# Performance work log

Hardware: AMD Instinct MI355X
Metric: run time of the kernel (lower is better)

The kernel has to match this reference:

```python
import jax, jax.numpy as jnp
import numpy as np

# Config: AydinConfig(hidden_dim=1024, intermediate_dim=2048, num_experts=8, top_k=2)
E, H, I, K = 8, 1024, 2048, 2
B, S = 4, 2048


def setup_inputs() -> dict:
    key = jax.random.key(0)
    k1, k2, k3, k4 = jax.random.split(key, 4)
    x = jax.random.normal(k1, (B, S, H), dtype=jnp.float32)
    # nn.Linear(H, E, bias=False): weight shape (E, H), default init ~ U(-1/sqrt(H), 1/sqrt(H))
    router_w = jax.random.uniform(k2, (E, H), dtype=jnp.float32,
                                  minval=-1.0, maxval=1.0) / np.sqrt(H).astype(np.float32)
    # normal init, std=0.02 (reset_parameters)
    w13 = jax.random.normal(k3, (E, H, 2 * I), dtype=jnp.float32) * 0.02
    w2 = jax.random.normal(k4, (E, I, H), dtype=jnp.float32) * 0.02
    return {"x": x, "router_w": router_w, "w13": w13, "w2": w2}


def reference(x, router_w, w13, w2):
    # Router: logits (B,S,E) -> softmax -> top-k with renormalized weights
    logits = jnp.einsum('bsh,eh->bse', x, router_w)
    probs = jax.nn.softmax(logits, axis=-1)
    weights, indices = jax.lax.top_k(probs, K)            # (B,S,K)
    weights = weights / (weights.sum(axis=-1, keepdims=True) + 1e-6)
    # Expert SwiGLU, computed densely over all experts then gathered.
    # Same math as the torch per-token weight gather, but avoids the
    # (B,S,K,H,2I) gathered-weight blowup.
    h13 = jnp.einsum('bsh,ehi->bsei', x, w13)             # (B,S,E,2I)
    gate, up = jnp.split(h13, 2, axis=-1)                 # (B,S,E,I) each
    h = jax.nn.silu(gate) * up
    y = jnp.einsum('bsei,eih->bseh', h, w2)               # (B,S,E,H)
    # Gather top-k expert outputs and combine with routing weights
    y_sel = jnp.take_along_axis(y, indices[..., None], axis=2)  # (B,S,K,H)
    return (y_sel * weights[..., None]).sum(axis=2)       # (B,S,H)
```

## Files before the change

### kernel.cpp

```cpp
#include <hip/hip_runtime.h>
#include <hip/hip_bf16.h>
#include <math.h>

#define NEXP 8
#define HD 1024
#define ID 2048
#define NTOK 8192
#define NROWS 16384

typedef __bf16 bf16_t;
typedef __bf16 bf16x8 __attribute__((ext_vector_type(8)));
typedef float f32x4 __attribute__((ext_vector_type(4)));

#define BM 128
#define BK 32
#define MAXT 160

__device__ __forceinline__ void gl16(const void* g, void* l) {
    __builtin_amdgcn_global_load_lds(
        (const __attribute__((address_space(1))) unsigned int*)g,
        (__attribute__((address_space(3))) unsigned int*)l, 16, 0, 0);
}

__global__ __launch_bounds__(256)
void router_kernel(const float* __restrict__ x, const float* __restrict__ rw,
                   bf16_t* __restrict__ xb, int* __restrict__ topk_idx,
                   float* __restrict__ topk_w)
{
    const int t = blockIdx.x;
    const int tid = threadIdx.x;
    const float4 xv = ((const float4*)(x + (size_t)t * HD))[tid];
    float acc[NEXP];
#pragma unroll
    for (int e = 0; e < NEXP; ++e) {
        const float4 w4 = ((const float4*)(rw + e * HD))[tid];
        acc[e] = xv.x * w4.x + xv.y * w4.y + xv.z * w4.z + xv.w * w4.w;
    }
    bf16_t tmp[4] = {(bf16_t)xv.x, (bf16_t)xv.y, (bf16_t)xv.z, (bf16_t)xv.w};
    *(uint2*)(xb + (size_t)t * HD + tid * 4) = *(const uint2*)tmp;

    __shared__ float red[4][NEXP];
    const int lane = tid & 63, wv = tid >> 6;
#pragma unroll
    for (int e = 0; e < NEXP; ++e) {
        float v = acc[e];
#pragma unroll
        for (int off = 32; off >= 1; off >>= 1) v += __shfl_down(v, off, 64);
        if (lane == 0) red[wv][e] = v;
    }
    __syncthreads();
    if (tid == 0) {
        float lg[NEXP], mx = -1e30f;
#pragma unroll
        for (int e = 0; e < NEXP; ++e) {
            lg[e] = red[0][e] + red[1][e] + red[2][e] + red[3][e];
            mx = fmaxf(mx, lg[e]);
        }
        float p[NEXP], s = 0.f;
#pragma unroll
        for (int e = 0; e < NEXP; ++e) { p[e] = __expf(lg[e] - mx); s += p[e]; }
        const float inv = 1.f / s;
#pragma unroll
        for (int e = 0; e < NEXP; ++e) p[e] *= inv;
        int i0 = 0; float p0 = p[0];
#pragma unroll
        for (int e = 1; e < NEXP; ++e) if (p[e] > p0) { p0 = p[e]; i0 = e; }
        int i1 = -1; float p1 = -1.f;
#pragma unroll
        for (int e = 0; e < NEXP; ++e) if (e != i0 && p[e] > p1) { p1 = p[e]; i1 = e; }
        const float d = 1.f / (p0 + p1 + 1e-6f);
        topk_idx[t * 2 + 0] = i0; topk_idx[t * 2 + 1] = i1;
        topk_w[t * 2 + 0] = p0 * d; topk_w[t * 2 + 1] = p1 * d;
    }
}

__global__ __launch_bounds__(256)
void count_kernel(const int* __restrict__ topk_idx, int* __restrict__ counts)
{
    __shared__ int lc[NEXP];
    const int tid = threadIdx.x;
    if (tid < NEXP) lc[tid] = 0;
    __syncthreads();
    const int t = blockIdx.x * 256 + tid;
    atomicAdd(&lc[topk_idx[t * 2 + 0]], 1);
    atomicAdd(&lc[topk_idx[t * 2 + 1]], 1);
    __syncthreads();
    if (tid < NEXP) atomicAdd(&counts[tid], lc[tid]);
}

__global__ void scan_kernel(const int* __restrict__ counts, int* __restrict__ offsets,
                            int* __restrict__ cursor, unsigned* __restrict__ tile_map)
{
    __shared__ int tb[NEXP + 1];
    if (threadIdx.x == 0) {
        int s = 0, tacc = 0;
        for (int e = 0; e < NEXP; ++e) {
            offsets[e] = s; cursor[e] = s; s += counts[e];
            tb[e] = tacc; tacc += (counts[e] + BM - 1) / BM;
        }
        tb[NEXP] = tacc;
    }
    __syncthreads();
    for (int i = threadIdx.x; i < MAXT; i += 64) {
        unsigned v = 0xFFFFFFFFu;
#pragma unroll
        for (int e = 0; e < NEXP; ++e)
            if (i >= tb[e] && i < tb[e + 1]) v = ((unsigned)e << 16) | (unsigned)(i - tb[e]);
        tile_map[i] = v;
    }
}

__global__ __launch_bounds__(256)
void scatter_kernel(const int* __restrict__ topk_idx, const float* __restrict__ topk_w,
                    int* __restrict__ cursor, int* __restrict__ token_list,
                    float* __restrict__ row_w, int* __restrict__ row_pos)
{
    __shared__ int lc[NEXP], gbase[NEXP];
    const int tid = threadIdx.x;
    if (tid < NEXP) lc[tid] = 0;
    __syncthreads();
    const int t = blockIdx.x * 256 + tid;
    const int e0 = topk_idx[t * 2 + 0], e1 = topk_idx[t * 2 + 1];
    const int lp0 = atomicAdd(&lc[e0], 1);
    const int lp1 = atomicAdd(&lc[e1], 1);
    __syncthreads();
    if (tid < NEXP) gbase[tid] = atomicAdd(&cursor[tid], lc[tid]);
    __syncthreads();
    const int p0 = gbase[e0] + lp0, p1 = gbase[e1] + lp1;
    token_list[p0] = t; row_w[p0] = topk_w[t * 2 + 0]; row_pos[t * 2 + 0] = p0;
    token_list[p1] = t; row_w[p1] = topk_w[t * 2 + 1]; row_pos[t * 2 + 1] = p1;
}

__global__ __launch_bounds__(256)
void precast_kernel(const float* __restrict__ src, bf16_t* __restrict__ dst,
                    int K, int N)
{
    const int e = blockIdx.z;
    src += (size_t)e * K * N;
    dst += (size_t)e * K * N;
    const int n0 = blockIdx.x * 64, k0 = blockIdx.y * 64;
    __shared__ float tile[64][65];
    const int tid = threadIdx.x;
    const int tx = (tid & 15) * 4, ty = tid >> 4;
#pragma unroll
    for (int p = 0; p < 4; ++p) {
        const float4 v = *(const float4*)(src + (size_t)(k0 + ty + p * 16) * N + n0 + tx);
        tile[ty + p * 16][tx + 0] = v.x;
        tile[ty + p * 16][tx + 1] = v.y;
        tile[ty + p * 16][tx + 2] = v.z;
        tile[ty + p * 16][tx + 3] = v.w;
    }
    __syncthreads();
    const int n = tid >> 2, kc = (tid & 3) * 16;
    bf16_t outv[16];
#pragma unroll
    for (int j = 0; j < 16; ++j) outv[j] = (bf16_t)tile[kc + j][n];
    bf16_t* d = dst + (size_t)(n0 + n) * K + k0 + kc;
    *(uint4*)d = *(uint4*)outv;
    *(uint4*)(d + 8) = *((uint4*)outv + 1);
}

__global__ __launch_bounds__(256)
void gemm1_kernel(const bf16_t* __restrict__ xb, const bf16_t* __restrict__ w13b,
                  const int* __restrict__ offsets, const int* __restrict__ counts,
                  const int* __restrict__ token_list,
                  const unsigned* __restrict__ tile_map, bf16_t* __restrict__ hbuf)
{
    const unsigned tm = tile_map[blockIdx.y];
    if (tm == 0xFFFFFFFFu) return;
    const int e = (int)(tm >> 16), mt = (int)(tm & 0xFFFFu);
    const int rows = counts[e];
    const int row_base = offsets[e];
    const int r0 = mt * BM;
    const int n0 = blockIdx.x * 64;

    __shared__ alignas(16) bf16_t As[128][32];
    __shared__ alignas(16) bf16_t Bg[64][32];
    __shared__ alignas(16) bf16_t Bu[64][32];

    const int tid = threadIdx.x;
    const int lane = tid & 63;
    const int wv = tid >> 6, wr = wv >> 1, wc = wv & 1;
    const int ln15 = lane & 15, q = lane >> 4;

    const int srow = tid >> 2, scol = (tid & 3) * 8;
    int gr0 = row_base + r0 + srow;      if (gr0 > NROWS - 1) gr0 = NROWS - 1;
    int gr1 = row_base + r0 + 64 + srow; if (gr1 > NROWS - 1) gr1 = NROWS - 1;
    const bf16_t* a0 = xb + (size_t)token_list[gr0] * HD + scol;
    const bf16_t* a1 = xb + (size_t)token_list[gr1] * HD + scol;
    const bf16_t* wb = w13b + (size_t)e * HD * (2 * ID);
    const bf16_t* bg = wb + (size_t)(n0 + srow) * HD + scol;
    const bf16_t* bu = wb + (size_t)(ID + n0 + srow) * HD + scol;
    bf16_t* const d_a0 = &As[0][0] + tid * 8;
    bf16_t* const d_a1 = &As[64][0] + tid * 8;
    bf16_t* const d_bg = &Bg[0][0] + tid * 8;
    bf16_t* const d_bu = &Bu[0][0] + tid * 8;

    f32x4 accG[4][2], accU[4][2];
#pragma unroll
    for (int i = 0; i < 4; ++i)
#pragma unroll
        for (int j = 0; j < 2; ++j)
#pragma unroll
            for (int c = 0; c < 4; ++c) { accG[i][j][c] = 0.f; accU[i][j][c] = 0.f; }

    for (int k0 = 0; k0 < HD; k0 += BK) {
        gl16(a0, d_a0); gl16(a1, d_a1); gl16(bg, d_bg); gl16(bu, d_bu);
        a0 += BK; a1 += BK; bg += BK; bu += BK;
        __syncthreads();

        bf16x8 af[4], bgf[2], buf_[2];
#pragma unroll
        for (int i = 0; i < 4; ++i)
            af[i] = *(const bf16x8*)&As[wr * 64 + i * 16 + ln15][q * 8];
#pragma unroll
        for (int j = 0; j < 2; ++j) {
            bgf[j]  = *(const bf16x8*)&Bg[wc * 32 + j * 16 + ln15][q * 8];
            buf_[j] = *(const bf16x8*)&Bu[wc * 32 + j * 16 + ln15][q * 8];
        }
#pragma unroll
        for (int i = 0; i < 4; ++i)
#pragma unroll
            for (int j = 0; j < 2; ++j) {
                accG[i][j] = __builtin_amdgcn_mfma_f32_16x16x32_bf16(af[i], bgf[j], accG[i][j], 0, 0, 0);
                accU[i][j] = __builtin_amdgcn_mfma_f32_16x16x32_bf16(af[i], buf_[j], accU[i][j], 0, 0, 0);
            }
        __syncthreads();
    }

#pragma unroll
    for (int i = 0; i < 4; ++i) {
#pragma unroll
        for (int reg = 0; reg < 4; ++reg) {
            const int rr = wr * 64 + i * 16 + q * 4 + reg;
            if (r0 + rr < rows) {
                bf16_t* dst = hbuf + (size_t)(row_base + r0 + rr) * ID + n0 + wc * 32 + ln15;
#pragma unroll
                for (int j = 0; j < 2; ++j) {
                    const float g = accG[i][j][reg], u = accU[i][j][reg];
                    dst[j * 16] = (bf16_t)((g / (1.f + __expf(-g))) * u);
                }
            }
        }
    }
}

__global__ __launch_bounds__(256)
void gemm2_kernel(const bf16_t* __restrict__ hbuf, const bf16_t* __restrict__ w2b,
                  const int* __restrict__ offsets, const int* __restrict__ counts,
                  const float* __restrict__ row_w,
                  const unsigned* __restrict__ tile_map, float* __restrict__ ybuf)
{
    const unsigned tm = tile_map[blockIdx.y];
    if (tm == 0xFFFFFFFFu) return;
    const int e = (int)(tm >> 16), mt = (int)(tm & 0xFFFFu);
    const int rows = counts[e];
    const int row_base = offsets[e];
    const int r0 = mt * BM;
    const int n0 = blockIdx.x * 128;

    __shared__ alignas(16) bf16_t As[128][32];
    __shared__ alignas(16) bf16_t Bs[128][32];
    __shared__ float rww_s[128];

    const int tid = threadIdx.x;
    if (tid < 128) {
        int gr = row_base + r0 + tid; if (gr > NROWS - 1) gr = NROWS - 1;
        rww_s[tid] = row_w[gr];
    }
    const int lane = tid & 63;
    const int wv = tid >> 6, wr = wv >> 1, wc = wv & 1;
    const int ln15 = lane & 15, q = lane >> 4;

    const int srow = tid >> 2, scol = (tid & 3) * 8;
    int gr0 = row_base + r0 + srow;      if (gr0 > NROWS - 1) gr0 = NROWS - 1;
    int gr1 = row_base + r0 + 64 + srow; if (gr1 > NROWS - 1) gr1 = NROWS - 1;
    const bf16_t* a0 = hbuf + (size_t)gr0 * ID + scol;
    const bf16_t* a1 = hbuf + (size_t)gr1 * ID + scol;
    const bf16_t* w2e = w2b + (size_t)e * ID * HD;
    const bf16_t* b0 = w2e + (size_t)(n0 + srow) * ID + scol;
    const bf16_t* b1 = w2e + (size_t)(n0 + 64 + srow) * ID + scol;
    bf16_t* const d_a0 = &As[0][0] + tid * 8;
    bf16_t* const d_a1 = &As[64][0] + tid * 8;
    bf16_t* const d_b0 = &Bs[0][0] + tid * 8;
    bf16_t* const d_b1 = &Bs[64][0] + tid * 8;

    f32x4 acc[4][4];
#pragma unroll
    for (int i = 0; i < 4; ++i)
#pragma unroll
        for (int j = 0; j < 4; ++j)
#pragma unroll
            for (int c = 0; c < 4; ++c) acc[i][j][c] = 0.f;

    for (int k0 = 0; k0 < ID; k0 += BK) {
        gl16(a0, d_a0); gl16(a1, d_a1); gl16(b0, d_b0); gl16(b1, d_b1);
        a0 += BK; a1 += BK; b0 += BK; b1 += BK;
        __syncthreads();

        bf16x8 af[4], bf_[4];
#pragma unroll
        for (int i = 0; i < 4; ++i)
            af[i] = *(const bf16x8*)&As[wr * 64 + i * 16 + ln15][q * 8];
#pragma unroll
        for (int j = 0; j < 4; ++j)
            bf_[j] = *(const bf16x8*)&Bs[wc * 64 + j * 16 + ln15][q * 8];
#pragma unroll
        for (int i = 0; i < 4; ++i)
#pragma unroll
            for (int j = 0; j < 4; ++j)
                acc[i][j] = __builtin_amdgcn_mfma_f32_16x16x32_bf16(af[i], bf_[j], acc[i][j], 0, 0, 0);
        __syncthreads();
    }

#pragma unroll
    for (int i = 0; i < 4; ++i) {
#pragma unroll
        for (int reg = 0; reg < 4; ++reg) {
            const int rr = wr * 64 + i * 16 + q * 4 + reg;
            if (r0 + rr < rows) {
                const float w = rww_s[rr];
                float* dst = ybuf + (size_t)(row_base + r0 + rr) * HD + n0 + wc * 64 + ln15;
#pragma unroll
                for (int j = 0; j < 4; ++j)
                    dst[j * 16] = acc[i][j][reg] * w;
            }
        }
    }
}

__global__ __launch_bounds__(256)
void combine_kernel(const float* __restrict__ ybuf, const int* __restrict__ row_pos,
                    float* __restrict__ out)
{
    const int t = blockIdx.x;
    const int p0 = row_pos[t * 2 + 0], p1 = row_pos[t * 2 + 1];
    const float4 a = ((const float4*)(ybuf + (size_t)p0 * HD))[threadIdx.x];
    const float4 b = ((const float4*)(ybuf + (size_t)p1 * HD))[threadIdx.x];
    float4 o; o.x = a.x + b.x; o.y = a.y + b.y; o.z = a.z + b.z; o.w = a.w + b.w;
    ((float4*)(out + (size_t)t * HD))[threadIdx.x] = o;
}

extern "C" void kernel_launch(void* const* d_in, const int* in_sizes, int n_in,
                              void* d_out, int out_size, void* d_ws, size_t ws_size,
                              hipStream_t stream) {
    const float* x   = (const float*)d_in[0];
    const float* rw  = (const float*)d_in[1];
    const float* w13 = (const float*)d_in[2];
    const float* w2  = (const float*)d_in[3];
    float* out = (float*)d_out;

    char* ws = (char*)d_ws;
    int*      counts     = (int*)(ws + 0);
    int*      cursor     = (int*)(ws + 64);
    int*      offsets    = (int*)(ws + 128);
    int*      topk_idx   = (int*)(ws + 256);
    float*    topk_w     = (float*)(ws + 256 + 1 * 65536);
    int*      token_list = (int*)(ws + 256 + 2 * 65536);
    float*    row_w      = (float*)(ws + 256 + 3 * 65536);
    int*      row_pos    = (int*)(ws + 256 + 4 * 65536);
    unsigned* tile_map   = (unsigned*)(ws + 256 + 5 * 65536);
    const size_t MB = 1024 * 1024;
    bf16_t* xb   = (bf16_t*)(ws + 1 * MB);
    bf16_t* hbuf = (bf16_t*)(ws + 17 * MB);
    bf16_t* w13b = (bf16_t*)(ws + 81 * MB);
    float*  ybuf = (float*)(ws + 81 * MB);
    bf16_t* w2b  = (bf16_t*)(ws + 145 * MB);

    hipMemsetAsync(ws, 0, 256, stream);

    dim3 gp1(2 * ID / 64, HD / 64, NEXP);
    precast_kernel<<<gp1, 256, 0, stream>>>(w13, w13b, HD, 2 * ID);
    dim3 gp2(HD / 64, ID / 64, NEXP);
    precast_kernel<<<gp2, 256, 0, stream>>>(w2, w2b, ID, HD);

    router_kernel<<<NTOK, 256, 0, stream>>>(x, rw, xb, topk_idx, topk_w);
    count_kernel<<<NTOK / 256, 256, 0, stream>>>(topk_idx, counts);
    scan_kernel<<<1, 64, 0, stream>>>(counts, offsets, cursor, tile_map);
    scatter_kernel<<<NTOK / 256, 256, 0, stream>>>(topk_idx, topk_w, cursor,
                                                   token_list, row_w, row_pos);

    dim3 g1(2 * ID / 128, MAXT);
    gemm1_kernel<<<g1, 256, 0, stream>>>(xb, w13b, offsets, counts, token_list,
                                         tile_map, hbuf);
    dim3 g2(HD / 128, MAXT);
    gemm2_kernel<<<g2, 256, 0, stream>>>(hbuf, w2b, offsets, counts, row_w,
                                         tile_map, ybuf);
    combine_kernel<<<NTOK, 256, 0, stream>>>(ybuf, row_pos, out);
}
```

Measured before the change: 601.4 us.

## Enlarge MoE GEMM tiles, double-buffer LDS, swizzle layout, interleave gate/up weights

Both expert GEMMs move to 512-thread blocks with larger output tiles: 256x256 for gemm1 and 128x256 for gemm2. The LDS loads are now double-buffered so the next K-slice is fetched while MFMAs run on the current one, and an XOR swizzle on the LDS chunk index is meant to cut bank conflicts. A new precast kernel interleaves the gate and up columns of w13 in 32-column groups, so one B tile carries both halves and SiLU*up is done in registers. The larger tiles mean more padding waste on partially filled per-expert tiles and higher register pressure for the 8x4 accumulators, which risks spills at 2 blocks per CU.

Result: slower. 647.2 us (+7.6%).

```diff
diff --git a/kernel.cpp b/kernel.cpp
--- a/kernel.cpp
+++ b/kernel.cpp
@@ -12,9 +12,9 @@
 typedef __bf16 bf16x8 __attribute__((ext_vector_type(8)));
 typedef float f32x4 __attribute__((ext_vector_type(4)));
 
-#define BM 128
 #define BK 32
-#define MAXT 160
+#define MAXT1 72
+#define MAXT2 136
 
 __device__ __forceinline__ void gl16(const void* g, void* l) {
     __builtin_amdgcn_global_load_lds(
@@ -89,24 +89,33 @@
 }
 
 __global__ void scan_kernel(const int* __restrict__ counts, int* __restrict__ offsets,
-                            int* __restrict__ cursor, unsigned* __restrict__ tile_map)
-{
-    __shared__ int tb[NEXP + 1];
+                            int* __restrict__ cursor,
+                            unsigned* __restrict__ map256, unsigned* __restrict__ map128)
+{
+    __shared__ int tb2[NEXP + 1], tb1[NEXP + 1];
     if (threadIdx.x == 0) {
-        int s = 0, tacc = 0;
+        int s = 0, t2 = 0, t1 = 0;
         for (int e = 0; e < NEXP; ++e) {
             offsets[e] = s; cursor[e] = s; s += counts[e];
-            tb[e] = tacc; tacc += (counts[e] + BM - 1) / BM;
-        }
-        tb[NEXP] = tacc;
-    }
-    __syncthreads();
-    for (int i = threadIdx.x; i < MAXT; i += 64) {
+            tb2[e] = t2; t2 += (counts[e] + 255) >> 8;
+            tb1[e] = t1; t1 += (counts[e] + 127) >> 7;
+        }
+        tb2[NEXP] = t2; tb1[NEXP] = t1;
+    }
+    __syncthreads();
+    for (int i = threadIdx.x; i < MAXT1; i += 64) {
         unsigned v = 0xFFFFFFFFu;
 #pragma unroll
         for (int e = 0; e < NEXP; ++e)
-            if (i >= tb[e] && i < tb[e + 1]) v = ((unsigned)e << 16) | (unsigned)(i - tb[e]);
-        tile_map[i] = v;
+            if (i >= tb2[e] && i < tb2[e + 1]) v = ((unsigned)e << 16) | (unsigned)(i - tb2[e]);
+        map256[i] = v;
+    }
+    for (int i = threadIdx.x; i < MAXT2; i += 64) {
+        unsigned v = 0xFFFFFFFFu;
+#pragma unroll
+        for (int e = 0; e < NEXP; ++e)
+            if (i >= tb1[e] && i < tb1[e + 1]) v = ((unsigned)e << 16) | (unsigned)(i - tb1[e]);
+        map128[i] = v;
     }
 }
 
@@ -161,7 +170,41 @@
 }
 
 __global__ __launch_bounds__(256)
-void gemm1_kernel(const bf16_t* __restrict__ xb, const bf16_t* __restrict__ w13b,
+void precast13_kernel(const float* __restrict__ src, bf16_t* __restrict__ dst)
+{
+    const int e = blockIdx.z;
+    src += (size_t)e * HD * (2 * ID);
+    dst += (size_t)e * HD * (2 * ID);
+    const int g = blockIdx.x;
+    const int k0 = blockIdx.y * 64;
+    __shared__ float tile[64][65];
+    const int tid = threadIdx.x;
+    const int tx = (tid & 7) * 4, ty = tid >> 3;
+#pragma unroll
+    for (int s = 0; s < 2; ++s) {
+        const int cbase = s == 0 ? g * 32 : 2048 + g * 32;
+#pragma unroll
+        for (int p = 0; p < 2; ++p) {
+            const int kk = ty + p * 32;
+            const float4 v = *(const float4*)(src + (size_t)(k0 + kk) * (2 * ID) + cbase + tx);
+            tile[kk][s * 32 + tx + 0] = v.x;
+            tile[kk][s * 32 + tx + 1] = v.y;
+            tile[kk][s * 32 + tx + 2] = v.z;
+            tile[kk][s * 32 + tx + 3] = v.w;
+        }
+    }
+    __syncthreads();
+    const int m = tid >> 2, kc = (tid & 3) * 16;
+    bf16_t outv[16];
+#pragma unroll
+    for (int j = 0; j < 16; ++j) outv[j] = (bf16_t)tile[kc + j][m];
+    bf16_t* d = dst + (size_t)(g * 64 + m) * HD + k0 + kc;
+    *(uint4*)d = *(uint4*)outv;
+    *(uint4*)(d + 8) = *((uint4*)outv + 1);
+}
+
+__global__ __launch_bounds__(512, 2)
+void gemm1_kernel(const bf16_t* __restrict__ xb, const bf16_t* __restrict__ w13i,
                   const int* __restrict__ offsets, const int* __restrict__ counts,
                   const int* __restrict__ token_list,
                   const unsigned* __restrict__ tile_map, bf16_t* __restrict__ hbuf)
@@ -171,73 +214,81 @@
     const int e = (int)(tm >> 16), mt = (int)(tm & 0xFFFFu);
     const int rows = counts[e];
     const int row_base = offsets[e];
-    const int r0 = mt * BM;
-    const int n0 = blockIdx.x * 64;
-
-    __shared__ alignas(16) bf16_t As[128][32];
-    __shared__ alignas(16) bf16_t Bg[64][32];
-    __shared__ alignas(16) bf16_t Bu[64][32];
-
-    const int tid = threadIdx.x;
-    const int lane = tid & 63;
-    const int wv = tid >> 6, wr = wv >> 1, wc = wv & 1;
+    const int r0 = mt * 256;
+    const int N0 = blockIdx.x * 256;
+
+    __shared__ alignas(16) bf16_t As[2][256][32];
+    __shared__ alignas(16) bf16_t Bs[2][256][32];
+
+    const int tid = threadIdx.x;
+    const int lane = tid & 63, wv = tid >> 6;
+    const int wr = wv >> 2, wc = wv & 3;
     const int ln15 = lane & 15, q = lane >> 4;
-
-    const int srow = tid >> 2, scol = (tid & 3) * 8;
-    int gr0 = row_base + r0 + srow;      if (gr0 > NROWS - 1) gr0 = NROWS - 1;
-    int gr1 = row_base + r0 + 64 + srow; if (gr1 > NROWS - 1) gr1 = NROWS - 1;
-    const bf16_t* a0 = xb + (size_t)token_list[gr0] * HD + scol;
-    const bf16_t* a1 = xb + (size_t)token_list[gr1] * HD + scol;
-    const bf16_t* wb = w13b + (size_t)e * HD * (2 * ID);
-    const bf16_t* bg = wb + (size_t)(n0 + srow) * HD + scol;
-    const bf16_t* bu = wb + (size_t)(ID + n0 + srow) * HD + scol;
-    bf16_t* const d_a0 = &As[0][0] + tid * 8;
-    bf16_t* const d_a1 = &As[64][0] + tid * 8;
-    bf16_t* const d_bg = &Bg[0][0] + tid * 8;
-    bf16_t* const d_bu = &Bu[0][0] + tid * 8;
-
-    f32x4 accG[4][2], accU[4][2];
-#pragma unroll
-    for (int i = 0; i < 4; ++i)
-#pragma unroll
-        for (int j = 0; j < 2; ++j)
-#pragma unroll
-            for (int c = 0; c < 4; ++c) { accG[i][j][c] = 0.f; accU[i][j][c] = 0.f; }
-
-    for (int k0 = 0; k0 < HD; k0 += BK) {
-        gl16(a0, d_a0); gl16(a1, d_a1); gl16(bg, d_bg); gl16(bu, d_bu);
-        a0 += BK; a1 += BK; bg += BK; bu += BK;
+    const int cs = (q ^ ((ln15 >> 1) & 3)) * 8;
+
+    const int srow = tid >> 2;
+    const int schunk = ((tid & 3) ^ ((tid >> 3) & 3)) * 8;
+    int gr0 = row_base + r0 + srow;       if (gr0 > NROWS - 1) gr0 = NROWS - 1;
+    int gr1 = row_base + r0 + 128 + srow; if (gr1 > NROWS - 1) gr1 = NROWS - 1;
+    const bf16_t* a0 = xb + (size_t)token_list[gr0] * HD + schunk;
+    const bf16_t* a1 = xb + (size_t)token_list[gr1] * HD + schunk;
+    const bf16_t* b0 = w13i + ((size_t)e * (2 * ID) + N0 + srow) * HD + schunk;
+    const bf16_t* b1 = b0 + (size_t)128 * HD;
+
+    f32x4 acc[8][4];
+#pragma unroll
+    for (int i = 0; i < 8; ++i)
+#pragma unroll
+        for (int j = 0; j < 4; ++j)
+#pragma unroll
+            for (int c = 0; c < 4; ++c) acc[i][j][c] = 0.f;
+
+    gl16(a0, &As[0][0][0] + tid * 8);
+    gl16(a1, &As[0][128][0] + tid * 8);
+    gl16(b0, &Bs[0][0][0] + tid * 8);
+    gl16(b1, &Bs[0][128][0] + tid * 8);
+    __syncthreads();
+
+    const int NT = HD / BK;
+    int cur = 0;
+    for (int t = 0; t < NT; ++t) {
+        if (t + 1 < NT) {
+            const int k = (t + 1) * BK;
+            const int nb = cur ^ 1;
+            gl16(a0 + k, &As[nb][0][0] + tid * 8);
+            gl16(a1 + k, &As[nb][128][0] + tid * 8);
+            gl16(b0 + k, &Bs[nb][0][0] + tid * 8);
+            gl16(b1 + k, &Bs[nb][128][0] + tid * 8);
+        }
+        bf16x8 af[8], bfr[4];
+#pragma unroll
+        for (int i = 0; i < 8; ++i)
+            af[i] = *(const bf16x8*)&As[cur][wr * 128 + i * 16 + ln15][cs];
+#pragma unroll
+        for (int j = 0; j < 4; ++j)
+            bfr[j] = *(const bf16x8*)&Bs[cur][wc * 64 + j * 16 + ln15][cs];
+        __builtin_amdgcn_s_setprio(1);
+#pragma unroll
+        for (int i = 0; i < 8; ++i)
+#pragma unroll
+            for (int j = 0; j < 4; ++j)
+                acc[i][j] = __builtin_amdgcn_mfma_f32_16x16x32_bf16(af[i], bfr[j], acc[i][j], 0, 0, 0);
+        __builtin_amdgcn_s_setprio(0);
         __syncthreads();
-
-        bf16x8 af[4], bgf[2], buf_[2];
-#pragma unroll
-        for (int i = 0; i < 4; ++i)
-            af[i] = *(const bf16x8*)&As[wr * 64 + i * 16 + ln15][q * 8];
-#pragma unroll
-        for (int j = 0; j < 2; ++j) {
-            bgf[j]  = *(const bf16x8*)&Bg[wc * 32 + j * 16 + ln15][q * 8];
-            buf_[j] = *(const bf16x8*)&Bu[wc * 32 + j * 16 + ln15][q * 8];
-        }
-#pragma unroll
-        for (int i = 0; i < 4; ++i)
-#pragma unroll
-            for (int j = 0; j < 2; ++j) {
-                accG[i][j] = __builtin_amdgcn_mfma_f32_16x16x32_bf16(af[i], bgf[j], accG[i][j], 0, 0, 0);
-                accU[i][j] = __builtin_amdgcn_mfma_f32_16x16x32_bf16(af[i], buf_[j], accU[i][j], 0, 0, 0);
-            }
-        __syncthreads();
-    }
-
-#pragma unroll
-    for (int i = 0; i < 4; ++i) {
+        cur ^= 1;
+    }
+
+    const int hbase = (N0 >> 1) + wc * 32;
+#pragma unroll
+    for (int i = 0; i < 8; ++i) {
 #pragma unroll
         for (int reg = 0; reg < 4; ++reg) {
-            const int rr = wr * 64 + i * 16 + q * 4 + reg;
+            const int rr = wr * 128 + i * 16 + q * 4 + reg;
             if (r0 + rr < rows) {
-                bf16_t* dst = hbuf + (size_t)(row_base + r0 + rr) * ID + n0 + wc * 32 + ln15;
+                bf16_t* dst = hbuf + (size_t)(row_base + r0 + rr) * ID + hbase + ln15;
 #pragma unroll
                 for (int j = 0; j < 2; ++j) {
-                    const float g = accG[i][j][reg], u = accU[i][j][reg];
+                    const float g = acc[i][j][reg], u = acc[i][j + 2][reg];
                     dst[j * 16] = (bf16_t)((g / (1.f + __expf(-g))) * u);
                 }
             }
@@ -245,7 +296,7 @@
     }
 }
 
-__global__ __launch_bounds__(256)
+__global__ __launch_bounds__(512, 2)
 void gemm2_kernel(const bf16_t* __restrict__ hbuf, const bf16_t* __restrict__ w2b,
                   const int* __restrict__ offsets, const int* __restrict__ counts,
                   const float* __restrict__ row_w,
@@ -256,11 +307,11 @@
     const int e = (int)(tm >> 16), mt = (int)(tm & 0xFFFFu);
     const int rows = counts[e];
     const int row_base = offsets[e];
-    const int r0 = mt * BM;
-    const int n0 = blockIdx.x * 128;
-
-    __shared__ alignas(16) bf16_t As[128][32];
-    __shared__ alignas(16) bf16_t Bs[128][32];
+    const int r0 = mt * 128;
+    const int N0 = blockIdx.x * 256;
+
+    __shared__ alignas(16) bf16_t As[2][128][32];
+    __shared__ alignas(16) bf16_t Bs[2][256][32];
     __shared__ float rww_s[128];
 
     const int tid = threadIdx.x;
@@ -268,22 +319,17 @@
         int gr = row_base + r0 + tid; if (gr > NROWS - 1) gr = NROWS - 1;
         rww_s[tid] = row_w[gr];
     }
-    const int lane = tid & 63;
-    const int wv = tid >> 6, wr = wv >> 1, wc = wv & 1;
+    const int lane = tid & 63, wv = tid >> 6;
+    const int wr = wv >> 2, wc = wv & 3;
     const int ln15 = lane & 15, q = lane >> 4;
-
-    const int srow = tid >> 2, scol = (tid & 3) * 8;
-    int gr0 = row_base + r0 + srow;      if (gr0 > NROWS - 1) gr0 = NROWS - 1;
-    int gr1 = row_base + r0 + 64 + srow; if (gr1 > NROWS - 1) gr1 = NROWS - 1;
-    const bf16_t* a0 = hbuf + (size_t)gr0 * ID + scol;
-    const bf16_t* a1 = hbuf + (size_t)gr1 * ID + scol;
-    const bf16_t* w2e = w2b + (size_t)e * ID * HD;
-    const bf16_t* b0 = w2e + (size_t)(n0 + srow) * ID + scol;
-    const bf16_t* b1 = w2e + (size_t)(n0 + 64 + srow) * ID + scol;
-    bf16_t* const d_a0 = &As[0][0] + tid * 8;
-    bf16_t* const d_a1 = &As[64][0] + tid * 8;
-    bf16_t* const d_b0 = &Bs[0][0] + tid * 8;
-    bf16_t* const d_b1 = &Bs[64][0] + tid * 8;
+    const int cs = (q ^ ((ln15 >> 1) & 3)) * 8;
+
+    const int srow = tid >> 2;
+    const int schunk = ((tid & 3) ^ ((tid >> 3) & 3)) * 8;
+    int gr0 = row_base + r0 + srow; if (gr0 > NROWS - 1) gr0 = NROWS - 1;
+    const bf16_t* a0 = hbuf + (size_t)gr0 * ID + schunk;
+    const bf16_t* b0 = w2b + ((size_t)e * HD + N0 + srow) * ID + schunk;
+    const bf16_t* b1 = b0 + (size_t)128 * ID;
 
     f32x4 acc[4][4];
 #pragma unroll
@@ -293,24 +339,37 @@
 #pragma unroll
             for (int c = 0; c < 4; ++c) acc[i][j][c] = 0.f;
 
-    for (int k0 = 0; k0 < ID; k0 += BK) {
-        gl16(a0, d_a0); gl16(a1, d_a1); gl16(b0, d_b0); gl16(b1, d_b1);
-        a0 += BK; a1 += BK; b0 += BK; b1 += BK;
+    gl16(a0, &As[0][0][0] + tid * 8);
+    gl16(b0, &Bs[0][0][0] + tid * 8);
+    gl16(b1, &Bs[0][128][0] + tid * 8);
+    __syncthreads();
+
+    const int NT = ID / BK;
+    int cur = 0;
+    for (int t = 0; t < NT; ++t) {
+        if (t + 1 < NT) {
+            const int k = (t + 1) * BK;
+            const int nb = cur ^ 1;
+            gl16(a0 + k, &As[nb][0][0] + tid * 8);
+            gl16(b0 + k, &Bs[nb][0][0] + tid * 8);
+            gl16(b1 + k, &Bs[nb][128][0] + tid * 8);
+        }
+        bf16x8 af[4], bfr[4];
+#pragma unroll
+        for (int i = 0; i < 4; ++i)
+            af[i] = *(const bf16x8*)&As[cur][wr * 64 + i * 16 + ln15][cs];
+#pragma unroll
+        for (int j = 0; j < 4; ++j)
+            bfr[j] = *(const bf16x8*)&Bs[cur][wc * 64 + j * 16 + ln15][cs];
+        __builtin_amdgcn_s_setprio(1);
+#pragma unroll
+        for (int i = 0; i < 4; ++i)
+#pragma unroll
+            for (int j = 0; j < 4; ++j)
+                acc[i][j] = __builtin_amdgcn_mfma_f32_16x16x32_bf16(af[i], bfr[j], acc[i][j], 0, 0, 0);
+        __builtin_amdgcn_s_setprio(0);
         __syncthreads();
-
-        bf16x8 af[4], bf_[4];
-#pragma unroll
-        for (int i = 0; i < 4; ++i)
-            af[i] = *(const bf16x8*)&As[wr * 64 + i * 16 + ln15][q * 8];
-#pragma unroll
-        for (int j = 0; j < 4; ++j)
-            bf_[j] = *(const bf16x8*)&Bs[wc * 64 + j * 16 + ln15][q * 8];
-#pragma unroll
-        for (int i = 0; i < 4; ++i)
-#pragma unroll
-            for (int j = 0; j < 4; ++j)
-                acc[i][j] = __builtin_amdgcn_mfma_f32_16x16x32_bf16(af[i], bf_[j], acc[i][j], 0, 0, 0);
-        __syncthreads();
+        cur ^= 1;
     }
 
 #pragma unroll
@@ -320,7 +379,7 @@
             const int rr = wr * 64 + i * 16 + q * 4 + reg;
             if (r0 + rr < rows) {
                 const float w = rww_s[rr];
-                float* dst = ybuf + (size_t)(row_base + r0 + rr) * HD + n0 + wc * 64 + ln15;
+                float* dst = ybuf + (size_t)(row_base + r0 + rr) * HD + N0 + wc * 64 + ln15;
 #pragma unroll
                 for (int j = 0; j < 4; ++j)
                     dst[j * 16] = acc[i][j][reg] * w;
@@ -359,32 +418,33 @@
     int*      token_list = (int*)(ws + 256 + 2 * 65536);
     float*    row_w      = (float*)(ws + 256 + 3 * 65536);
     int*      row_pos    = (int*)(ws + 256 + 4 * 65536);
-    unsigned* tile_map   = (unsigned*)(ws + 256 + 5 * 65536);
+    unsigned* map256     = (unsigned*)(ws + 256 + 5 * 65536);
+    unsigned* map128     = (unsigned*)(ws + 256 + 6 * 65536);
     const size_t MB = 1024 * 1024;
     bf16_t* xb   = (bf16_t*)(ws + 1 * MB);
     bf16_t* hbuf = (bf16_t*)(ws + 17 * MB);
-    bf16_t* w13b = (bf16_t*)(ws + 81 * MB);
+    bf16_t* w13i = (bf16_t*)(ws + 81 * MB);
     float*  ybuf = (float*)(ws + 81 * MB);
     bf16_t* w2b  = (bf16_t*)(ws + 145 * MB);
 
     hipMemsetAsync(ws, 0, 256, stream);
 
-    dim3 gp1(2 * ID / 64, HD / 64, NEXP);
-    precast_kernel<<<gp1, 256, 0, stream>>>(w13, w13b, HD, 2 * ID);
+    dim3 gp1(64, HD / 64, NEXP);
+    precast13_kernel<<<gp1, 256, 0, stream>>>(w13, w13i);
     dim3 gp2(HD / 64, ID / 64, NEXP);
     precast_kernel<<<gp2, 256, 0, stream>>>(w2, w2b, ID, HD);
 
     router_kernel<<<NTOK, 256, 0, stream>>>(x, rw, xb, topk_idx, topk_w);
     count_kernel<<<NTOK / 256, 256, 0, stream>>>(topk_idx, counts);
-    scan_kernel<<<1, 64, 0, stream>>>(counts, offsets, cursor, tile_map);
+    scan_kernel<<<1, 64, 0, stream>>>(counts, offsets, cursor, map256, map128);
     scatter_kernel<<<NTOK / 256, 256, 0, stream>>>(topk_idx, topk_w, cursor,
                                                    token_list, row_w, row_pos);
 
-    dim3 g1(2 * ID / 128, MAXT);
-    gemm1_kernel<<<g1, 256, 0, stream>>>(xb, w13b, offsets, counts, token_list,
-                                         tile_map, hbuf);
-    dim3 g2(HD / 128, MAXT);
-    gemm2_kernel<<<g2, 256, 0, stream>>>(hbuf, w2b, offsets, counts, row_w,
-                                         tile_map, ybuf);
+    dim3 g1(2 * ID / 256, MAXT1);
+    gemm1_kernel<<<g1, 512, 0, stream>>>(xb, w13i, offsets, counts, token_list,
+                                         map256, hbuf);
+    dim3 g2(HD / 256, MAXT2);
+    gemm2_kernel<<<g2, 512, 0, stream>>>(hbuf, w2b, offsets, counts, row_w,
+                                         map128, ybuf);
     combine_kernel<<<NTOK, 256, 0, stream>>>(ybuf, row_pos, out);
 }
```

## Swizzle LDS tiles in expert GEMMs, fold expert counting into router, shrink tile grid

Applied to the files above, without the earlier changes.

Applies an XOR swizzle to the 16-byte column chunks written into shared memory and read back for MFMA operands in both expert GEMMs, aiming to remove LDS bank conflicts on the fragment reads. Expert counting moves into the router kernel as per-token global atomics, so the separate count kernel launch goes away. The maximum tile count drops from 160 to 136, which trims the number of idle blocks launched. The risk is heavier global atomic contention on the 8 counters, and a too-small tile bound if the routing turns out more imbalanced than expected.

Measured after the change: 817.5 us. 35.9% more time.

```diff
diff --git a/kernel.cpp b/kernel.cpp
--- a/kernel.cpp
+++ b/kernel.cpp
@@ -14,7 +14,7 @@
 
 #define BM 128
 #define BK 32
-#define MAXT 160
+#define MAXT 136
 
 __device__ __forceinline__ void gl16(const void* g, void* l) {
     __builtin_amdgcn_global_load_lds(
@@ -25,7 +25,7 @@
 __global__ __launch_bounds__(256)
 void router_kernel(const float* __restrict__ x, const float* __restrict__ rw,
                    bf16_t* __restrict__ xb, int* __restrict__ topk_idx,
-                   float* __restrict__ topk_w)
+                   float* __restrict__ topk_w, int* __restrict__ counts)
 {
     const int t = blockIdx.x;
     const int tid = threadIdx.x;
@@ -71,21 +71,9 @@
         const float d = 1.f / (p0 + p1 + 1e-6f);
         topk_idx[t * 2 + 0] = i0; topk_idx[t * 2 + 1] = i1;
         topk_w[t * 2 + 0] = p0 * d; topk_w[t * 2 + 1] = p1 * d;
-    }
-}
-
-__global__ __launch_bounds__(256)
-void count_kernel(const int* __restrict__ topk_idx, int* __restrict__ counts)
-{
-    __shared__ int lc[NEXP];
-    const int tid = threadIdx.x;
-    if (tid < NEXP) lc[tid] = 0;
-    __syncthreads();
-    const int t = blockIdx.x * 256 + tid;
-    atomicAdd(&lc[topk_idx[t * 2 + 0]], 1);
-    atomicAdd(&lc[topk_idx[t * 2 + 1]], 1);
-    __syncthreads();
-    if (tid < NEXP) atomicAdd(&counts[tid], lc[tid]);
+        atomicAdd(&counts[i0], 1);
+        atomicAdd(&counts[i1], 1);
+    }
 }
 
 __global__ void scan_kernel(const int* __restrict__ counts, int* __restrict__ offsets,
@@ -182,15 +170,17 @@
     const int lane = tid & 63;
     const int wv = tid >> 6, wr = wv >> 1, wc = wv & 1;
     const int ln15 = lane & 15, q = lane >> 4;
-
-    const int srow = tid >> 2, scol = (tid & 3) * 8;
+    const int cs = (q ^ ((ln15 >> 1) & 3)) * 8;
+
+    const int srow = tid >> 2;
+    const int schunk = ((tid & 3) ^ ((tid >> 3) & 3)) * 8;
     int gr0 = row_base + r0 + srow;      if (gr0 > NROWS - 1) gr0 = NROWS - 1;
     int gr1 = row_base + r0 + 64 + srow; if (gr1 > NROWS - 1) gr1 = NROWS - 1;
-    const bf16_t* a0 = xb + (size_t)token_list[gr0] * HD + scol;
-    const bf16_t* a1 = xb + (size_t)token_list[gr1] * HD + scol;
+    const bf16_t* a0 = xb + (size_t)token_list[gr0] * HD + schunk;
+    const bf16_t* a1 = xb + (size_t)token_list[gr1] * HD + schunk;
     const bf16_t* wb = w13b + (size_t)e * HD * (2 * ID);
-    const bf16_t* bg = wb + (size_t)(n0 + srow) * HD + scol;
-    const bf16_t* bu = wb + (size_t)(ID + n0 + srow) * HD + scol;
+    const bf16_t* bg = wb + (size_t)(n0 + srow) * HD + schunk;
+    const bf16_t* bu = wb + (size_t)(ID + n0 + srow) * HD + schunk;
     bf16_t* const d_a0 = &As[0][0] + tid * 8;
     bf16_t* const d_a1 = &As[64][0] + tid * 8;
     bf16_t* const d_bg = &Bg[0][0] + tid * 8;
@@ -212,11 +202,11 @@
         bf16x8 af[4], bgf[2], buf_[2];
 #pragma unroll
         for (int i = 0; i < 4; ++i)
-            af[i] = *(const bf16x8*)&As[wr * 64 + i * 16 + ln15][q * 8];
+            af[i] = *(const bf16x8*)&As[wr * 64 + i * 16 + ln15][cs];
 #pragma unroll
         for (int j = 0; j < 2; ++j) {
-            bgf[j]  = *(const bf16x8*)&Bg[wc * 32 + j * 16 + ln15][q * 8];
-            buf_[j] = *(const bf16x8*)&Bu[wc * 32 + j * 16 + ln15][q * 8];
+            bgf[j]  = *(const bf16x8*)&Bg[wc * 32 + j * 16 + ln15][cs];
+            buf_[j] = *(const bf16x8*)&Bu[wc * 32 + j * 16 + ln15][cs];
         }
 #pragma unroll
         for (int i = 0; i < 4; ++i)
@@ -271,15 +261,17 @@
     const int lane = tid & 63;
     const int wv = tid >> 6, wr = wv >> 1, wc = wv & 1;
     const int ln15 = lane & 15, q = lane >> 4;
-
-    const int srow = tid >> 2, scol = (tid & 3) * 8;
+    const int cs = (q ^ ((ln15 >> 1) & 3)) * 8;
+
+    const int srow = tid >> 2;
+    const int schunk = ((tid & 3) ^ ((tid >> 3) & 3)) * 8;
     int gr0 = row_base + r0 + srow;      if (gr0 > NROWS - 1) gr0 = NROWS - 1;
     int gr1 = row_base + r0 + 64 + srow; if (gr1 > NROWS - 1) gr1 = NROWS - 1;
-    const bf16_t* a0 = hbuf + (size_t)gr0 * ID + scol;
-    const bf16_t* a1 = hbuf + (size_t)gr1 * ID + scol;
+    const bf16_t* a0 = hbuf + (size_t)gr0 * ID + schunk;
+    const bf16_t* a1 = hbuf + (size_t)gr1 * ID + schunk;
     const bf16_t* w2e = w2b + (size_t)e * ID * HD;
-    const bf16_t* b0 = w2e + (size_t)(n0 + srow) * ID + scol;
-    const bf16_t* b1 = w2e + (size_t)(n0 + 64 + srow) * ID + scol;
+    const bf16_t* b0 = w2e + (size_t)(n0 + srow) * ID + schunk;
+    const bf16_t* b1 = b0 + (size_t)64 * ID;
     bf16_t* const d_a0 = &As[0][0] + tid * 8;
     bf16_t* const d_a1 = &As[64][0] + tid * 8;
     bf16_t* const d_b0 = &Bs[0][0] + tid * 8;
@@ -301,10 +293,10 @@
         bf16x8 af[4], bf_[4];
 #pragma unroll
         for (int i = 0; i < 4; ++i)
-            af[i] = *(const bf16x8*)&As[wr * 64 + i * 16 + ln15][q * 8];
+            af[i] = *(const bf16x8*)&As[wr * 64 + i * 16 + ln15][cs];
 #pragma unroll
         for (int j = 0; j < 4; ++j)
-            bf_[j] = *(const bf16x8*)&Bs[wc * 64 + j * 16 + ln15][q * 8];
+            bf_[j] = *(const bf16x8*)&Bs[wc * 64 + j * 16 + ln15][cs];
 #pragma unroll
         for (int i = 0; i < 4; ++i)
 #pragma unroll
@@ -374,13 +366,12 @@
     dim3 gp2(HD / 64, ID / 64, NEXP);
     precast_kernel<<<gp2, 256, 0, stream>>>(w2, w2b, ID, HD);
 
-    router_kernel<<<NTOK, 256, 0, stream>>>(x, rw, xb, topk_idx, topk_w);
-    count_kernel<<<NTOK / 256, 256, 0, stream>>>(topk_idx, counts);
+    router_kernel<<<NTOK, 256, 0, stream>>>(x, rw, xb, topk_idx, topk_w, counts);
     scan_kernel<<<1, 64, 0, stream>>>(counts, offsets, cursor, tile_map);
     scatter_kernel<<<NTOK / 256, 256, 0, stream>>>(topk_idx, topk_w, cursor,
                                                    token_list, row_w, row_pos);
 
-    dim3 g1(2 * ID / 128, MAXT);
+    dim3 g1(ID / 64, MAXT);
     gemm1_kernel<<<g1, 256, 0, stream>>>(xb, w13b, offsets, counts, token_list,
                                          tile_map, hbuf);
     dim3 g2(HD / 128, MAXT);
```

## Fuse top-k combine into gemm2 via atomic scatter-add to output

Applied to the files above, without the earlier changes.

The gemm2 epilogue now atomically adds the weighted expert outputs straight into the token rows of the output. This removes the intermediate ybuf, the row_pos bookkeeping and the separate combine kernel, and the output is zeroed with a memset first. The maximum tile count is lowered from 160 to 136, which trims the number of idle blocks launched. Atomic float adds make the summation order nondeterministic and cost more per store than plain writes, and MAXT must still cover the worst-case per-expert padding or tiles will be dropped.

Measured after the change: 622.8 us. +3.6%, slower.

```diff
diff --git a/kernel.cpp b/kernel.cpp
--- a/kernel.cpp
+++ b/kernel.cpp
@@ -14,7 +14,7 @@
 
 #define BM 128
 #define BK 32
-#define MAXT 160
+#define MAXT 136
 
 __device__ __forceinline__ void gl16(const void* g, void* l) {
     __builtin_amdgcn_global_load_lds(
@@ -113,7 +113,7 @@
 __global__ __launch_bounds__(256)
 void scatter_kernel(const int* __restrict__ topk_idx, const float* __restrict__ topk_w,
                     int* __restrict__ cursor, int* __restrict__ token_list,
-                    float* __restrict__ row_w, int* __restrict__ row_pos)
+                    float* __restrict__ row_w)
 {
     __shared__ int lc[NEXP], gbase[NEXP];
     const int tid = threadIdx.x;
@@ -127,8 +127,8 @@
     if (tid < NEXP) gbase[tid] = atomicAdd(&cursor[tid], lc[tid]);
     __syncthreads();
     const int p0 = gbase[e0] + lp0, p1 = gbase[e1] + lp1;
-    token_list[p0] = t; row_w[p0] = topk_w[t * 2 + 0]; row_pos[t * 2 + 0] = p0;
-    token_list[p1] = t; row_w[p1] = topk_w[t * 2 + 1]; row_pos[t * 2 + 1] = p1;
+    token_list[p0] = t; row_w[p0] = topk_w[t * 2 + 0];
+    token_list[p1] = t; row_w[p1] = topk_w[t * 2 + 1];
 }
 
 __global__ __launch_bounds__(256)
@@ -248,8 +248,8 @@
 __global__ __launch_bounds__(256)
 void gemm2_kernel(const bf16_t* __restrict__ hbuf, const bf16_t* __restrict__ w2b,
                   const int* __restrict__ offsets, const int* __restrict__ counts,
-                  const float* __restrict__ row_w,
-                  const unsigned* __restrict__ tile_map, float* __restrict__ ybuf)
+                  const int* __restrict__ token_list, const float* __restrict__ row_w,
+                  const unsigned* __restrict__ tile_map, float* __restrict__ out)
 {
     const unsigned tm = tile_map[blockIdx.y];
     if (tm == 0xFFFFFFFFu) return;
@@ -262,11 +262,13 @@
     __shared__ alignas(16) bf16_t As[128][32];
     __shared__ alignas(16) bf16_t Bs[128][32];
     __shared__ float rww_s[128];
+    __shared__ int   tok_s[128];
 
     const int tid = threadIdx.x;
     if (tid < 128) {
         int gr = row_base + r0 + tid; if (gr > NROWS - 1) gr = NROWS - 1;
         rww_s[tid] = row_w[gr];
+        tok_s[tid] = token_list[gr];
     }
     const int lane = tid & 63;
     const int wv = tid >> 6, wr = wv >> 1, wc = wv & 1;
@@ -279,7 +281,7 @@
     const bf16_t* a1 = hbuf + (size_t)gr1 * ID + scol;
     const bf16_t* w2e = w2b + (size_t)e * ID * HD;
     const bf16_t* b0 = w2e + (size_t)(n0 + srow) * ID + scol;
-    const bf16_t* b1 = w2e + (size_t)(n0 + 64 + srow) * ID + scol;
+    const bf16_t* b1 = b0 + (size_t)64 * ID;
     bf16_t* const d_a0 = &As[0][0] + tid * 8;
     bf16_t* const d_a1 = &As[64][0] + tid * 8;
     bf16_t* const d_b0 = &Bs[0][0] + tid * 8;
@@ -320,25 +322,13 @@
             const int rr = wr * 64 + i * 16 + q * 4 + reg;
             if (r0 + rr < rows) {
                 const float w = rww_s[rr];
-                float* dst = ybuf + (size_t)(row_base + r0 + rr) * HD + n0 + wc * 64 + ln15;
+                float* dst = out + (size_t)tok_s[rr] * HD + n0 + wc * 64 + ln15;
 #pragma unroll
                 for (int j = 0; j < 4; ++j)
-                    dst[j * 16] = acc[i][j][reg] * w;
+                    atomicAdd(&dst[j * 16], acc[i][j][reg] * w);
             }
         }
     }
-}
-
-__global__ __launch_bounds__(256)
-void combine_kernel(const float* __restrict__ ybuf, const int* __restrict__ row_pos,
-                    float* __restrict__ out)
-{
-    const int t = blockIdx.x;
-    const int p0 = row_pos[t * 2 + 0], p1 = row_pos[t * 2 + 1];
-    const float4 a = ((const float4*)(ybuf + (size_t)p0 * HD))[threadIdx.x];
-    const float4 b = ((const float4*)(ybuf + (size_t)p1 * HD))[threadIdx.x];
-    float4 o; o.x = a.x + b.x; o.y = a.y + b.y; o.z = a.z + b.z; o.w = a.w + b.w;
-    ((float4*)(out + (size_t)t * HD))[threadIdx.x] = o;
 }
 
 extern "C" void kernel_launch(void* const* d_in, const int* in_sizes, int n_in,
@@ -358,16 +348,15 @@
     float*    topk_w     = (float*)(ws + 256 + 1 * 65536);
     int*      token_list = (int*)(ws + 256 + 2 * 65536);
     float*    row_w      = (float*)(ws + 256 + 3 * 65536);
-    int*      row_pos    = (int*)(ws + 256 + 4 * 65536);
-    unsigned* tile_map   = (unsigned*)(ws + 256 + 5 * 65536);
+    unsigned* tile_map   = (unsigned*)(ws + 256 + 4 * 65536);
     const size_t MB = 1024 * 1024;
     bf16_t* xb   = (bf16_t*)(ws + 1 * MB);
     bf16_t* hbuf = (bf16_t*)(ws + 17 * MB);
     bf16_t* w13b = (bf16_t*)(ws + 81 * MB);
-    float*  ybuf = (float*)(ws + 81 * MB);
     bf16_t* w2b  = (bf16_t*)(ws + 145 * MB);
 
     hipMemsetAsync(ws, 0, 256, stream);
+    hipMemsetAsync(d_out, 0, (size_t)out_size * sizeof(float), stream);
 
     dim3 gp1(2 * ID / 64, HD / 64, NEXP);
     precast_kernel<<<gp1, 256, 0, stream>>>(w13, w13b, HD, 2 * ID);
@@ -378,13 +367,12 @@
     count_kernel<<<NTOK / 256, 256, 0, stream>>>(topk_idx, counts);
     scan_kernel<<<1, 64, 0, stream>>>(counts, offsets, cursor, tile_map);
     scatter_kernel<<<NTOK / 256, 256, 0, stream>>>(topk_idx, topk_w, cursor,
-                                                   token_list, row_w, row_pos);
-
-    dim3 g1(2 * ID / 128, MAXT);
+                                                   token_list, row_w);
+
+    dim3 g1(ID / 64, MAXT);
     gemm1_kernel<<<g1, 256, 0, stream>>>(xb, w13b, offsets, counts, token_list,
                                          tile_map, hbuf);
     dim3 g2(HD / 128, MAXT);
-    gemm2_kernel<<<g2, 256, 0, stream>>>(hbuf, w2b, offsets, counts, row_w,
-                                         tile_map, ybuf);
-    combine_kernel<<<NTOK, 256, 0, stream>>>(ybuf, row_pos, out);
-}
+    gemm2_kernel<<<g2, 256, 0, stream>>>(hbuf, w2b, offsets, counts, token_list,
+                                         row_w, tile_map, out);
+}
```
